# Kernel tuning notes

Hardware: AMD Instinct MI355X
Metric: run time of the kernel (lower is better)

## Reference

```python
import jax, jax.numpy as jnp
import numpy as np

D = 2048      # d_model
H = 16        # n_heads
DH = D // H   # per-head dim = 128
L = 512       # kv_latent_dim
B, S = 2, 2048
EPS = 1e-5


def setup_inputs() -> dict:
    key = jax.random.key(0)
    ks = jax.random.split(key, 8)
    sc = lambda fan_in: 1.0 / np.sqrt(fan_in)
    return {
        "x": jax.random.normal(ks[0], (B, S, D), dtype=jnp.float32),
        # torch Linear weights: (out_features, in_features)
        "W_q":   jax.random.normal(ks[1], (D, D), dtype=jnp.float32) * sc(D),
        "W_dkv": jax.random.normal(ks[2], (L, D), dtype=jnp.float32) * sc(D),
        "W_uk":  jax.random.normal(ks[3], (D, L), dtype=jnp.float32) * sc(L),
        "W_uv":  jax.random.normal(ks[4], (D, L), dtype=jnp.float32) * sc(L),
        "W_o":   jax.random.normal(ks[5], (D, D), dtype=jnp.float32) * sc(D),
        "ln_w":  jnp.ones((L,), dtype=jnp.float32),
        "ln_b":  jnp.zeros((L,), dtype=jnp.float32),
    }


def _layer_norm(x, w, b):
    mu = jnp.mean(x, axis=-1, keepdims=True)
    var = jnp.mean(jnp.square(x - mu), axis=-1, keepdims=True)
    return (x - mu) * jax.lax.rsqrt(var + EPS) * w + b


def reference(x, W_q, W_dkv, W_uk, W_uv, W_o, ln_w, ln_b):
    b, s, d = x.shape
    # projections (torch Linear: x @ W.T)
    q = (x @ W_q.T).reshape(b, s, H, DH)                  # (B,S,H,dh)
    c_kv = _layer_norm(x @ W_dkv.T, ln_w, ln_b)           # (B,S_full,L); no cache -> S_full = S
    v = (c_kv @ W_uv.T).reshape(b, s, H, DH)              # (B,S_full,H,dh)
    # absorbed key weights: W_uk.weight viewed as (H, dh, L)
    k_w = W_uk.reshape(H, DH, L)
    # per-head absorbed matmul, vectorized over heads
    tmp = jnp.einsum('bshd,hdl->bhsl', q, k_w)            # (B,H,S,L)
    scores = jnp.einsum('bhsl,btl->bhst', tmp, c_kv) / np.sqrt(DH)
    # causal mask (past_length=0): allow t <= s
    causal = jnp.tril(jnp.ones((s, s), dtype=bool))
    scores = jnp.where(causal[None, None], scores, -jnp.inf)
    attn = jax.nn.softmax(scores, axis=-1)                # (B,H,S,S_full)
    ctx = jnp.einsum('bhst,bthd->bshd', attn, v)          # (B,S,H,dh)
    out = ctx.reshape(b, s, D) @ W_o.T
    return out, c_kv
```

## Files before the change

### kernel.cpp

```cpp
#include <hip/hip_runtime.h>

#define B_  2
#define S_  2048
#define D_  2048
#define H_  16
#define DH_ 128
#define L_  512
#define M_  (B_*S_)

typedef unsigned short u16;
typedef float f32x4 __attribute__((ext_vector_type(4)));
typedef short short8 __attribute__((ext_vector_type(8)));
typedef u16 u16x4 __attribute__((ext_vector_type(4)));
typedef u16 u16x8 __attribute__((ext_vector_type(8)));

__device__ inline float bf2f(u16 u) {
    union { unsigned int i; float f; } x; x.i = ((unsigned int)u) << 16; return x.f;
}
__device__ inline u16 f2bf(float f) {
    union { float f; unsigned int i; } x; x.f = f;
    unsigned int r = x.i + 0x7FFFu + ((x.i >> 16) & 1u);
    return (u16)(r >> 16);
}
__device__ inline f32x4 mfma16(short8 a, short8 b, f32x4 c) {
    return __builtin_amdgcn_mfma_f32_16x16x32_bf16(a, b, c, 0, 0, 0);
}

typedef const __attribute__((address_space(1))) unsigned int gu32;
typedef __attribute__((address_space(3))) unsigned int lu32;
__device__ inline void gload16(const u16* g, u16* l) {
    __builtin_amdgcn_global_load_lds((gu32*)g, (lu32*)l, 16, 0, 0);
}

template <typename T> __device__ inline void store1(T* p, float v);
template <> __device__ inline void store1<float>(float* p, float v) { *p = v; }
template <> __device__ inline void store1<u16>(u16* p, float v) { *p = f2bf(v); }

template <typename TC, int BM, int BN, int WAVES_M, int WAVES_N>
__global__ __launch_bounds__(256) void mgemm(const u16* __restrict__ A,
                                             const u16* __restrict__ Bm,
                                             TC* __restrict__ C,
                                             int N, int K) {
    constexpr int WM = BM / WAVES_M;
    constexpr int WN = BN / WAVES_N;
    constexpr int FM = WM / 16;
    constexpr int FN = WN / 16;
    constexpr int CA = (BM * 8) / 256;
    constexpr int CB = (BN * 8) / 256;

    const int tid = threadIdx.x;
    const int bn = blockIdx.x * BN, bm = blockIdx.y * BM;
    const int w = tid >> 6, l = tid & 63;
    const int wr = w / WAVES_N, wc = w % WAVES_N;
    const int g = l >> 4, ln16 = l & 15;

    __shared__ u16 A_lds[BM * 64];
    __shared__ u16 B_lds[BN * 64];

    f32x4 acc[FM][FN];
#pragma unroll
    for (int m = 0; m < FM; ++m)
#pragma unroll
        for (int n = 0; n < FN; ++n) acc[m][n] = {0.f, 0.f, 0.f, 0.f};

    for (int k0 = 0; k0 < K; k0 += 64) {
        __syncthreads();
#pragma unroll
        for (int i = 0; i < CA; ++i) {
            int ch = tid + i * 256;
            int row = ch % BM, ks = ch / BM;
            gload16(A + (size_t)(bm + row) * K + k0 + ks * 8, &A_lds[ch * 8]);
        }
#pragma unroll
        for (int i = 0; i < CB; ++i) {
            int ch = tid + i * 256;
            int row = ch % BN, ks = ch / BN;
            gload16(Bm + (size_t)(bn + row) * K + k0 + ks * 8, &B_lds[ch * 8]);
        }
        __syncthreads();

#pragma unroll
        for (int ko = 0; ko < 2; ++ko) {
            short8 af[FM], bf[FN];
#pragma unroll
            for (int m = 0; m < FM; ++m)
                af[m] = *reinterpret_cast<const short8*>(
                    &A_lds[((ko*4 + g) * BM + wr * WM + m * 16 + ln16) * 8]);
#pragma unroll
            for (int n = 0; n < FN; ++n)
                bf[n] = *reinterpret_cast<const short8*>(
                    &B_lds[((ko*4 + g) * BN + wc * WN + n * 16 + ln16) * 8]);
#pragma unroll
            for (int m = 0; m < FM; ++m)
#pragma unroll
                for (int n = 0; n < FN; ++n)
                    acc[m][n] = mfma16(af[m], bf[n], acc[m][n]);
        }
    }

#pragma unroll
    for (int m = 0; m < FM; ++m)
#pragma unroll
        for (int n = 0; n < FN; ++n)
#pragma unroll
            for (int r = 0; r < 4; ++r)
                store1<TC>(&C[(size_t)(bm + wr*WM + m*16 + g*4 + r) * N + bn + wc*WN + n*16 + ln16],
                           acc[m][n][r]);
}

__global__ __launch_bounds__(256) void ln_fused(const float* __restrict__ pre,
                                                const float* __restrict__ w,
                                                const float* __restrict__ bias,
                                                float* __restrict__ out,
                                                u16* __restrict__ out_bf) {
    const int row = blockIdx.x;
    const int tid = threadIdx.x;
    __shared__ float red[256];
    const size_t base = (size_t)row * L_;
    float x0 = pre[base + tid];
    float x1 = pre[base + tid + 256];
    red[tid] = x0 + x1;
    __syncthreads();
    for (int o = 128; o; o >>= 1) { if (tid < o) red[tid] += red[tid + o]; __syncthreads(); }
    float mu = red[0] * (1.0f / L_);
    __syncthreads();
    float d0 = x0 - mu, d1 = x1 - mu;
    red[tid] = d0 * d0 + d1 * d1;
    __syncthreads();
    for (int o = 128; o; o >>= 1) { if (tid < o) red[tid] += red[tid + o]; __syncthreads(); }
    float rstd = rsqrtf(red[0] * (1.0f / L_) + 1e-5f);
    float y0 = d0 * rstd * w[tid]       + bias[tid];
    float y1 = d1 * rstd * w[tid + 256] + bias[tid + 256];
    out[base + tid]          = y0;
    out[base + tid + 256]    = y1;
    out_bf[base + tid]       = f2bf(y0);
    out_bf[base + tid + 256] = f2bf(y1);
}

__global__ __launch_bounds__(256) void cvt_bf16(const float* __restrict__ in,
                                                u16* __restrict__ out) {
    size_t i = ((size_t)blockIdx.x * 256 + threadIdx.x) * 4;
    f32x4 v = *reinterpret_cast<const f32x4*>(&in[i]);
    u16x4 o; o[0]=f2bf(v[0]); o[1]=f2bf(v[1]); o[2]=f2bf(v[2]); o[3]=f2bf(v[3]);
    *reinterpret_cast<u16x4*>(&out[i]) = o;
}

__global__ __launch_bounds__(512) void flash_split(const u16* __restrict__ qb,
                                                   const u16* __restrict__ kmat,
                                                   const u16* __restrict__ vbf,
                                                   u16* __restrict__ opart,
                                                   float* __restrict__ ml) {
    const int c  = blockIdx.z;
    const int bx = blockIdx.x;
    int qt2;
    if (c == 0)      qt2 = bx;
    else if (c == 1) qt2 = (bx + 8) & 15;
    else             qt2 = (bx < 8) ? (14 - 2*bx) : (31 - 2*bx);
    const int hh = blockIdx.y;
    const int tid = threadIdx.x;
    const int w = tid >> 6, l = tid & 63;
    const int g = l >> 4, ln16 = l & 15;

    const int nt = 2*qt2 + 2;
    const int kt0   = (c * nt) / 3;
    const int ktend = ((c + 1) * nt) / 3;
    if (ktend <= kt0) {
        if (tid < 128) ml[(size_t)(c*16 + hh)*S_ + qt2*128 + tid] = -3e38f;
        return;
    }

    __shared__ u16 K_lds[8192];
    __shared__ char V_lds[16384];
    __shared__ char P_lds[16384];
    char* P_my = P_lds + w * 2048;

    short8 qreg[4];
    {
        const u16* qbase = qb + (size_t)(qt2*128 + w*16 + ln16) * D_ + hh * DH_ + g*8;
#pragma unroll
        for (int kc = 0; kc < 4; ++kc)
            qreg[kc] = *reinterpret_cast<const short8*>(qbase + kc*32);
    }

    float m_run = -3e38f, l_run = 0.f;
    f32x4 acc[8];
#pragma unroll
    for (int cb = 0; cb < 8; ++cb) acc[cb] = {0,0,0,0};

    const int sq = qt2*128 + w*16 + ln16;
    const float scale = 0.08838834764831845f;

    for (int kt = kt0; kt < ktend; ++kt) {
        __syncthreads();
        const u16* ksrc = kmat + (size_t)kt * 64 * D_ + hh * DH_;
#pragma unroll
        for (int i = 0; i < 2; ++i) {
            int ch = tid + i * 512;
            int row = ch & 63, ks = ch >> 6;
            gload16(ksrc + (size_t)row * D_ + ks * 8, &K_lds[ch * 8]);
        }
        {
            const u16* vsrc = vbf + (size_t)kt * 64 * D_ + hh * DH_;
            const int kv = tid & 63;
#pragma unroll
            for (int p = 0; p < 2; ++p) {
                int dg = (tid >> 6) + p * 8;
                u16x8 v8 = *reinterpret_cast<const u16x8*>(vsrc + (size_t)kv * D_ + dg*8);
#pragma unroll
                for (int j = 0; j < 8; ++j) {
                    int dv = dg*8 + j;
                    *reinterpret_cast<u16*>(V_lds + ((dv*128 + kv*2) ^ (j << 4))) = v8[j];
                }
            }
        }
        __syncthreads();

        f32x4 sacc[4];
#pragma unroll
        for (int a = 0; a < 4; ++a) sacc[a] = {0,0,0,0};
#pragma unroll
        for (int a = 0; a < 4; ++a) {
            const int row = a*16 + ln16;
#pragma unroll
            for (int kc = 0; kc < 4; ++kc) {
                short8 kf = *reinterpret_cast<const short8*>(&K_lds[((kc*4 + g)*64 + row) * 8]);
                sacc[a] = mfma16(kf, qreg[kc], sacc[a]);
            }
        }

        float p[4][4];
        float tmax = -3e38f;
#pragma unroll
        for (int a = 0; a < 4; ++a)
#pragma unroll
            for (int r = 0; r < 4; ++r) {
                int t = kt*64 + a*16 + g*4 + r;
                float v = (t <= sq) ? sacc[a][r] * scale : -3e38f;
                p[a][r] = v;
                tmax = fmaxf(tmax, v);
            }
        tmax = fmaxf(tmax, __shfl_xor(tmax, 16, 64));
        tmax = fmaxf(tmax, __shfl_xor(tmax, 32, 64));
        float m_new = fmaxf(m_run, tmax);
        float fac = __expf(m_run - m_new);
        float rsum = 0.f;
#pragma unroll
        for (int a = 0; a < 4; ++a)
#pragma unroll
            for (int r = 0; r < 4; ++r) {
                float e = __expf(p[a][r] - m_new);
                p[a][r] = e;
                rsum += e;
            }
        rsum += __shfl_xor(rsum, 16, 64);
        rsum += __shfl_xor(rsum, 32, 64);
        l_run = l_run * fac + rsum;
        m_run = m_new;

        {
            const int ps = (ln16 & 7) << 4;
#pragma unroll
            for (int a = 0; a < 4; ++a) {
                u16x4 quad;
#pragma unroll
                for (int r = 0; r < 4; ++r) quad[r] = f2bf(p[a][r]);
                *reinterpret_cast<u16x4*>(P_my + ((ln16*128 + a*32 + g*8) ^ ps)) = quad;
            }
        }
        float fr[4];
#pragma unroll
        for (int r = 0; r < 4; ++r) fr[r] = __shfl(fac, g*4 + r, 64);
#pragma unroll
        for (int cb = 0; cb < 8; ++cb)
#pragma unroll
            for (int r = 0; r < 4; ++r) acc[cb][r] *= fr[r];

#pragma unroll
        for (int kc2 = 0; kc2 < 2; ++kc2) {
            short8 pf = *reinterpret_cast<const short8*>(
                P_my + ((ln16*128 + kc2*64 + g*16) ^ ((ln16 & 7) << 4)));
#pragma unroll
            for (int cb = 0; cb < 8; ++cb) {
                const int dv = cb*16 + ln16;
                short8 vf = *reinterpret_cast<const short8*>(
                    V_lds + ((dv*128 + kc2*64 + g*16) ^ ((dv & 7) << 4)));
                acc[cb] = mfma16(pf, vf, acc[cb]);
            }
        }
    }

    float inv = 1.0f / l_run;
    float lse = m_run + __logf(l_run);
    float ir[4];
#pragma unroll
    for (int r = 0; r < 4; ++r) ir[r] = __shfl(inv, g*4 + r, 64);
#pragma unroll
    for (int cb = 0; cb < 8; ++cb)
#pragma unroll
        for (int r = 0; r < 4; ++r) {
            int q = qt2*128 + w*16 + g*4 + r;
            opart[((size_t)(c*16 + hh)*S_ + q)*128 + cb*16 + ln16] = f2bf(acc[cb][r] * ir[r]);
        }
    if (g == 0) ml[(size_t)(c*16 + hh)*S_ + qt2*128 + w*16 + ln16] = lse;
}

__global__ __launch_bounds__(256) void combine(const u16* __restrict__ opart,
                                               const float* __restrict__ ml,
                                               u16* __restrict__ ctx) {
    int t = blockIdx.x * 256 + threadIdx.x;
    int qh = t >> 4;
    int q = qh >> 4, hh = qh & 15;
    int dv0 = (t & 15) * 8;

    float ls[3], m = -3e38f;
#pragma unroll
    for (int c = 0; c < 3; ++c) {
        ls[c] = ml[(size_t)(c*16 + hh) * S_ + q];
        m = fmaxf(m, ls[c]);
    }
    float e[3], s = 0.f;
#pragma unroll
    for (int c = 0; c < 3; ++c) { e[c] = __expf(ls[c] - m); s += e[c]; }
    float is = 1.0f / s;

    float accv[8] = {};
#pragma unroll
    for (int c = 0; c < 3; ++c) {
        if (e[c] > 0.f) {
            u16x8 a = *reinterpret_cast<const u16x8*>(
                &opart[((size_t)(c*16 + hh)*S_ + q)*128 + dv0]);
#pragma unroll
            for (int j = 0; j < 8; ++j) accv[j] += e[c] * bf2f(a[j]);
        }
    }
    u16x8 o;
#pragma unroll
    for (int j = 0; j < 8; ++j) o[j] = f2bf(accv[j] * is);
    *reinterpret_cast<u16x8*>(&ctx[(size_t)q * D_ + hh * DH_ + dv0]) = o;
}

extern "C" void kernel_launch(void* const* d_in, const int* in_sizes, int n_in,
                              void* d_out, int out_size, void* d_ws, size_t ws_size,
                              hipStream_t stream) {
    const float* x    = (const float*)d_in[0];
    const float* Wq   = (const float*)d_in[1];
    const float* Wdkv = (const float*)d_in[2];
    const float* Wuk  = (const float*)d_in[3];
    const float* Wuv  = (const float*)d_in[4];
    const float* Wo   = (const float*)d_in[5];
    const float* lnw  = (const float*)d_in[6];
    const float* lnb  = (const float*)d_in[7];

    float* out = (float*)d_out;
    float* ckv = out + (size_t)M_ * D_;

    char* ws = (char*)d_ws;
    u16*   xb_bf   = (u16*)(ws);
    u16*   kmat    = (u16*)(ws);
    u16*   qb_bf   = (u16*)(ws + (size_t)16777216);
    u16*   ctx_all = (u16*)(ws + (size_t)16777216);
    u16*   vb_bf   = (u16*)(ws + (size_t)33554432);
    u16*   wo_bf   = (u16*)(ws + (size_t)33554432);
    u16*   ckv_bf  = (u16*)(ws + (size_t)41943040);
    u16*   wuv_bf  = (u16*)(ws + (size_t)46137344);

    char*  ob0     = (char*)d_out;
    u16*   wslot   = (u16*)ob0;
    float* ckvp    = (float*)(ob0 + 8388608);
    u16*   opart   = (u16*)d_out;
    float* ml      = (float*)(ob0 + 25165824);

    dim3 blk(256);

    cvt_bf16<<<dim3(8192), blk, 0, stream>>>(x, xb_bf);
    cvt_bf16<<<dim3(1024), blk, 0, stream>>>(Wdkv, wslot);
    mgemm<float,64,64,2,2><<<dim3(L_/64, M_/64), blk, 0, stream>>>(xb_bf, wslot, ckvp, L_, D_);
    ln_fused<<<dim3(M_), blk, 0, stream>>>(ckvp, lnw, lnb, ckv, ckv_bf);
    cvt_bf16<<<dim3(4096), blk, 0, stream>>>(Wq, wslot);
    mgemm<u16,128,128,2,2><<<dim3(D_/128, M_/128), blk, 0, stream>>>(xb_bf, wslot, qb_bf, D_, D_);
    cvt_bf16<<<dim3(1024), blk, 0, stream>>>(Wuv, wuv_bf);
    cvt_bf16<<<dim3(1024), blk, 0, stream>>>(Wuk, wslot);
    mgemm<u16,128,128,2,2><<<dim3(D_/128, M_/128), blk, 0, stream>>>(ckv_bf, wslot, kmat, D_, L_);

    for (int b = 0; b < B_; ++b) {
        const u16* qb_b    = qb_bf  + (size_t)b * S_ * D_;
        const u16* kmat_b  = kmat   + (size_t)b * S_ * D_;
        const u16* ckvbf_b = ckv_bf + (size_t)b * S_ * L_;
        u16*       ctx_b   = ctx_all + (size_t)b * S_ * D_;

        mgemm<u16,128,64,4,1><<<dim3(D_/64, S_/128), blk, 0, stream>>>(ckvbf_b, wuv_bf, vb_bf, D_, L_);

        flash_split<<<dim3(16, 16, 3), dim3(512), 0, stream>>>(
            qb_b, kmat_b, vb_bf, opart, ml);
        combine<<<dim3(2048), blk, 0, stream>>>(opart, ml, ctx_b);
    }

    cvt_bf16<<<dim3(4096), blk, 0, stream>>>(Wo, wo_bf);
    mgemm<float,128,128,2,2><<<dim3(D_/128, M_/128), blk, 0, stream>>>(ctx_all, wo_bf, out, D_, D_);
}
```

Measured before the change: 422.4 us.

## Write V transposed from the up-projection GEMM and async-load it into flash LDS

The V up-projection GEMM gains a transposed epilogue that writes V as (head*dh, S) in bf16 using 4-element vector stores. The flash attention kernel then fills its V tile in LDS with global_load_lds 16-byte async copies, keeping the XOR swizzle, in place of per-element scalar LDS transposes done in registers. This is meant to cut LDS store traffic and VALU work in the attention inner loop. In exchange the GEMM epilogue does strided global writes, which may coalesce less well.

Result: faster. 365.7 us, median of 2 (-13.4%).

```diff
diff --git a/kernel.cpp b/kernel.cpp
--- a/kernel.cpp
+++ b/kernel.cpp
@@ -36,11 +36,11 @@
 template <> __device__ inline void store1<float>(float* p, float v) { *p = v; }
 template <> __device__ inline void store1<u16>(u16* p, float v) { *p = f2bf(v); }
 
-template <typename TC, int BM, int BN, int WAVES_M, int WAVES_N>
+template <typename TC, int BM, int BN, int WAVES_M, int WAVES_N, bool TRANS>
 __global__ __launch_bounds__(256) void mgemm(const u16* __restrict__ A,
                                              const u16* __restrict__ Bm,
                                              TC* __restrict__ C,
-                                             int N, int K) {
+                                             int N, int K, int ldC) {
     constexpr int WM = BM / WAVES_M;
     constexpr int WN = BN / WAVES_N;
     constexpr int FM = WM / 16;
@@ -98,14 +98,28 @@
         }
     }
 
-#pragma unroll
-    for (int m = 0; m < FM; ++m)
-#pragma unroll
-        for (int n = 0; n < FN; ++n)
-#pragma unroll
-            for (int r = 0; r < 4; ++r)
-                store1<TC>(&C[(size_t)(bm + wr*WM + m*16 + g*4 + r) * N + bn + wc*WN + n*16 + ln16],
-                           acc[m][n][r]);
+    if constexpr (TRANS) {
+#pragma unroll
+        for (int m = 0; m < FM; ++m)
+#pragma unroll
+            for (int n = 0; n < FN; ++n) {
+                u16x4 q4;
+#pragma unroll
+                for (int r = 0; r < 4; ++r) q4[r] = f2bf(acc[m][n][r]);
+                *reinterpret_cast<u16x4*>(
+                    (u16*)C + (size_t)(bn + wc*WN + n*16 + ln16) * ldC
+                            + bm + wr*WM + m*16 + g*4) = q4;
+            }
+    } else {
+#pragma unroll
+        for (int m = 0; m < FM; ++m)
+#pragma unroll
+            for (int n = 0; n < FN; ++n)
+#pragma unroll
+                for (int r = 0; r < 4; ++r)
+                    store1<TC>(&C[(size_t)(bm + wr*WM + m*16 + g*4 + r) * ldC + bn + wc*WN + n*16 + ln16],
+                               acc[m][n][r]);
+    }
 }
 
 __global__ __launch_bounds__(256) void ln_fused(const float* __restrict__ pre,
@@ -147,7 +161,7 @@
 
 __global__ __launch_bounds__(512) void flash_split(const u16* __restrict__ qb,
                                                    const u16* __restrict__ kmat,
-                                                   const u16* __restrict__ vbf,
+                                                   const u16* __restrict__ vt,
                                                    u16* __restrict__ opart,
                                                    float* __restrict__ ml) {
     const int c  = blockIdx.z;
@@ -199,19 +213,13 @@
             int row = ch & 63, ks = ch >> 6;
             gload16(ksrc + (size_t)row * D_ + ks * 8, &K_lds[ch * 8]);
         }
-        {
-            const u16* vsrc = vbf + (size_t)kt * 64 * D_ + hh * DH_;
-            const int kv = tid & 63;
-#pragma unroll
-            for (int p = 0; p < 2; ++p) {
-                int dg = (tid >> 6) + p * 8;
-                u16x8 v8 = *reinterpret_cast<const u16x8*>(vsrc + (size_t)kv * D_ + dg*8);
-#pragma unroll
-                for (int j = 0; j < 8; ++j) {
-                    int dv = dg*8 + j;
-                    *reinterpret_cast<u16*>(V_lds + ((dv*128 + kv*2) ^ (j << 4))) = v8[j];
-                }
-            }
+        const u16* vsrc = vt + (size_t)(hh * DH_) * S_ + kt * 64;
+#pragma unroll
+        for (int i = 0; i < 2; ++i) {
+            int ch = tid + i * 512;
+            int dv = ch >> 3, c16 = ch & 7;
+            int srcblk = c16 ^ (dv & 7);
+            gload16(vsrc + (size_t)dv * S_ + srcblk * 8, (u16*)V_lds + ch * 8);
         }
         __syncthreads();
 
@@ -359,7 +367,7 @@
     u16*   kmat    = (u16*)(ws);
     u16*   qb_bf   = (u16*)(ws + (size_t)16777216);
     u16*   ctx_all = (u16*)(ws + (size_t)16777216);
-    u16*   vb_bf   = (u16*)(ws + (size_t)33554432);
+    u16*   vt      = (u16*)(ws + (size_t)33554432);
     u16*   wo_bf   = (u16*)(ws + (size_t)33554432);
     u16*   ckv_bf  = (u16*)(ws + (size_t)41943040);
     u16*   wuv_bf  = (u16*)(ws + (size_t)46137344);
@@ -374,13 +382,13 @@
 
     cvt_bf16<<<dim3(8192), blk, 0, stream>>>(x, xb_bf);
     cvt_bf16<<<dim3(1024), blk, 0, stream>>>(Wdkv, wslot);
-    mgemm<float,64,64,2,2><<<dim3(L_/64, M_/64), blk, 0, stream>>>(xb_bf, wslot, ckvp, L_, D_);
+    mgemm<float,64,64,2,2,false><<<dim3(L_/64, M_/64), blk, 0, stream>>>(xb_bf, wslot, ckvp, L_, D_, L_);
     ln_fused<<<dim3(M_), blk, 0, stream>>>(ckvp, lnw, lnb, ckv, ckv_bf);
     cvt_bf16<<<dim3(4096), blk, 0, stream>>>(Wq, wslot);
-    mgemm<u16,128,128,2,2><<<dim3(D_/128, M_/128), blk, 0, stream>>>(xb_bf, wslot, qb_bf, D_, D_);
+    mgemm<u16,128,128,2,2,false><<<dim3(D_/128, M_/128), blk, 0, stream>>>(xb_bf, wslot, qb_bf, D_, D_, D_);
     cvt_bf16<<<dim3(1024), blk, 0, stream>>>(Wuv, wuv_bf);
     cvt_bf16<<<dim3(1024), blk, 0, stream>>>(Wuk, wslot);
-    mgemm<u16,128,128,2,2><<<dim3(D_/128, M_/128), blk, 0, stream>>>(ckv_bf, wslot, kmat, D_, L_);
+    mgemm<u16,128,128,2,2,false><<<dim3(D_/128, M_/128), blk, 0, stream>>>(ckv_bf, wslot, kmat, D_, L_, D_);
 
     for (int b = 0; b < B_; ++b) {
         const u16* qb_b    = qb_bf  + (size_t)b * S_ * D_;
@@ -388,13 +396,13 @@
         const u16* ckvbf_b = ckv_bf + (size_t)b * S_ * L_;
         u16*       ctx_b   = ctx_all + (size_t)b * S_ * D_;
 
-        mgemm<u16,128,64,4,1><<<dim3(D_/64, S_/128), blk, 0, stream>>>(ckvbf_b, wuv_bf, vb_bf, D_, L_);
+        mgemm<u16,128,64,4,1,true><<<dim3(D_/64, S_/128), blk, 0, stream>>>(ckvbf_b, wuv_bf, vt, D_, L_, S_);
 
         flash_split<<<dim3(16, 16, 3), dim3(512), 0, stream>>>(
-            qb_b, kmat_b, vb_bf, opart, ml);
+            qb_b, kmat_b, vt, opart, ml);
         combine<<<dim3(2048), blk, 0, stream>>>(opart, ml, ctx_b);
     }
 
     cvt_bf16<<<dim3(4096), blk, 0, stream>>>(Wo, wo_bf);
-    mgemm<float,128,128,2,2><<<dim3(D_/128, M_/128), blk, 0, stream>>>(ctx_all, wo_bf, out, D_, D_);
-}
+    mgemm<float,128,128,2,2,false><<<dim3(D_/128, M_/128), blk, 0, stream>>>(ctx_all, wo_bf, out, D_, D_, D_);
+}
```
